# Kernel tuning notes

Hardware: AMD Instinct MI355X
Metric: run time of the kernel (lower is better)

## Reference

```python
import jax, jax.numpy as jnp
import numpy as np
import math

PHI = (1.0 + math.sqrt(5.0)) / 2.0
LUT_SIZE = 4096
D_MODEL = 2048
BATCH = 8192
TWO_PI = 2.0 * math.pi


def lut_sin_cos(theta, sin_table, cos_table):
    """LUT-based sin/cos with linear interpolation over [0, 2*pi)."""
    n = sin_table.shape[0]
    pos = jnp.mod(theta, TWO_PI) * (n / TWO_PI)        # [B, D] in [0, n)
    i0f = jnp.floor(pos)
    frac = pos - i0f
    i0 = i0f.astype(jnp.int32) % n
    i1 = (i0 + 1) % n
    s = sin_table[i0] * (1.0 - frac) + sin_table[i1] * frac
    c = cos_table[i0] * (1.0 - frac) + cos_table[i1] * frac
    return s, c


def setup_inputs() -> dict:
    key = jax.random.key(0)
    ks = jax.random.split(key, 6)
    x_real = jax.random.normal(ks[0], (BATCH, D_MODEL), dtype=jnp.float32)
    x_imag = jax.random.normal(ks[1], (BATCH, D_MODEL), dtype=jnp.float32)
    t = jax.random.uniform(ks[2], (BATCH,), dtype=jnp.float32)
    memory_real = jnp.zeros((BATCH, D_MODEL), dtype=jnp.float32)
    memory_imag = jnp.zeros((BATCH, D_MODEL), dtype=jnp.float32)
    w_trigger = jax.random.normal(ks[3], (D_MODEL,), dtype=jnp.float32) * 0.02
    b_trigger = jnp.zeros((D_MODEL,), dtype=jnp.float32)
    w_state = jax.random.normal(ks[4], (D_MODEL,), dtype=jnp.float32) * 0.02
    b_state = jnp.zeros((D_MODEL,), dtype=jnp.float32)
    k = jnp.asarray(3.0, dtype=jnp.float32)
    grid = jnp.arange(LUT_SIZE, dtype=jnp.float32) * (TWO_PI / LUT_SIZE)
    sin_table = jnp.sin(grid)
    cos_table = jnp.cos(grid)
    return dict(x_real=x_real, x_imag=x_imag, t=t,
                memory_real=memory_real, memory_imag=memory_imag,
                w_trigger=w_trigger, b_trigger=b_trigger,
                w_state=w_state, b_state=b_state, k=k,
                sin_table=sin_table, cos_table=cos_table)


def reference(x_real, x_imag, t, memory_real, memory_imag,
              w_trigger, b_trigger, w_state, b_state, k,
              sin_table, cos_table):
    scale = math.sqrt(x_real.shape[-1])
    t_phi = t[:, None] * PHI                                  # [B, 1]

    # trigger phase
    wl_trigger = 1.0 + jnp.abs(w_trigger)
    theta_tr = x_real / wl_trigger + b_trigger + t_phi
    theta_ti = x_imag / wl_trigger + b_trigger + t_phi
    sin_tr, cos_tr = lut_sin_cos(theta_tr, sin_table, cos_table)
    sin_ti, cos_ti = lut_sin_cos(theta_ti, sin_table, cos_table)
    trigger_real = cos_tr * cos_ti - sin_tr * sin_ti
    trigger_imag = cos_tr * sin_ti + sin_tr * cos_ti

    # interference -> exponential decay gate
    interference_raw = jnp.sum(trigger_real * x_real + trigger_imag * x_imag, axis=-1)
    interference_clamped = jnp.clip(interference_raw / scale, -1.0, 1.0)
    x_inv = (1.0 - interference_clamped) / 2.0
    k_eff = jnp.abs(k) + 0.1
    alpha = jnp.exp(-k_eff * x_inv)[:, None]                  # [B, 1]

    # blend with (detached) memory, then re-evolve
    blended_real = alpha * x_real + (1.0 - alpha) * memory_real
    blended_imag = alpha * x_imag + (1.0 - alpha) * memory_imag
    wl_state = 1.0 + jnp.abs(w_state)
    theta_sr = blended_real / wl_state + b_state + t_phi
    theta_si = blended_imag / wl_state + b_state + t_phi
    sin_sr, cos_sr = lut_sin_cos(theta_sr, sin_table, cos_table)
    sin_si, cos_si = lut_sin_cos(theta_si, sin_table, cos_table)
    evolved_real = cos_sr * cos_si - sin_sr * sin_si
    evolved_imag = cos_sr * sin_si + sin_sr * cos_si
    return evolved_real, evolved_imag
```

## Files before the change

### kernel.cpp

```cpp
#include <hip/hip_runtime.h>

#define DMODEL   2048
#define NTHREADS 256

__device__ __forceinline__ void fast_sincos(float theta, float& s, float& c) {
    const float INV_TWO_PI = 0.15915494309189535f;
    float r  = theta * INV_TWO_PI;
    float rr = r - floorf(r);
#if __has_builtin(__builtin_amdgcn_sinf) && __has_builtin(__builtin_amdgcn_cosf)
    s = __builtin_amdgcn_sinf(rr);
    c = __builtin_amdgcn_cosf(rr);
#else
    s = __sinf(rr * 6.283185307179586f);
    c = __cosf(rr * 6.283185307179586f);
#endif
}

__device__ __forceinline__ float fast_rcp(float x) {
#if __has_builtin(__builtin_amdgcn_rcpf)
    return __builtin_amdgcn_rcpf(x);
#else
    return 1.0f / x;
#endif
}

__global__ __launch_bounds__(NTHREADS)
void liquid_echo_kernel(const float* __restrict__ x_real,
                        const float* __restrict__ x_imag,
                        const float* __restrict__ tvec,
                        const float* __restrict__ memory_real,
                        const float* __restrict__ memory_imag,
                        const float* __restrict__ w_trigger,
                        const float* __restrict__ b_trigger,
                        const float* __restrict__ w_state,
                        const float* __restrict__ b_state,
                        const float* __restrict__ kptr,
                        float* __restrict__ out,
                        size_t imag_off)
{
    __shared__ float red[NTHREADS / 64];

    const int tid = threadIdx.x;
    const int row = blockIdx.x;

    const float t_phi = tvec[row] * 1.6180339887498948f;
    const int c0 = tid * 4;
    const int c1 = (DMODEL / 2) + tid * 4;
    const size_t rb = (size_t)row * DMODEL;

    float4 xr0 = *(const float4*)(x_real + rb + c0);
    float4 xr1 = *(const float4*)(x_real + rb + c1);
    float4 xi0 = *(const float4*)(x_imag + rb + c0);
    float4 xi1 = *(const float4*)(x_imag + rb + c1);
    float4 wt0 = *(const float4*)(w_trigger + c0);
    float4 wt1 = *(const float4*)(w_trigger + c1);
    float4 bt0 = *(const float4*)(b_trigger + c0);
    float4 bt1 = *(const float4*)(b_trigger + c1);

    float xrv[8] = {xr0.x, xr0.y, xr0.z, xr0.w, xr1.x, xr1.y, xr1.z, xr1.w};
    float xiv[8] = {xi0.x, xi0.y, xi0.z, xi0.w, xi1.x, xi1.y, xi1.z, xi1.w};
    float wtv[8] = {wt0.x, wt0.y, wt0.z, wt0.w, wt1.x, wt1.y, wt1.z, wt1.w};
    float btv[8] = {bt0.x, bt0.y, bt0.z, bt0.w, bt1.x, bt1.y, bt1.z, bt1.w};

    float sxy[8];
    float partial = 0.0f;
    #pragma unroll
    for (int j = 0; j < 8; ++j) {
        float iw   = fast_rcp(1.0f + fabsf(wtv[j]));
        float base = btv[j] + t_phi;
        sxy[j]     = xrv[j] + xiv[j];
        float ths  = fmaf(sxy[j], iw, base + base);
        float s, c;
        fast_sincos(ths, s, c);
        partial = fmaf(c, xrv[j], partial);
        partial = fmaf(s, xiv[j], partial);
    }

    float4 mr0 = *(const float4*)(memory_real + rb + c0);
    float4 mr1 = *(const float4*)(memory_real + rb + c1);
    float4 mi0 = *(const float4*)(memory_imag + rb + c0);
    float4 mi1 = *(const float4*)(memory_imag + rb + c1);
    float4 ws0 = *(const float4*)(w_state + c0);
    float4 ws1 = *(const float4*)(w_state + c1);
    float4 bs0 = *(const float4*)(b_state + c0);
    float4 bs1 = *(const float4*)(b_state + c1);

    #pragma unroll
    for (int off = 32; off > 0; off >>= 1)
        partial += __shfl_down(partial, off, 64);
    if ((tid & 63) == 0) red[tid >> 6] = partial;
    __syncthreads();

    float tot   = red[0] + red[1] + red[2] + red[3];
    float ic    = tot * (1.0f / 45.254833995939045f);
    ic          = fminf(1.0f, fmaxf(-1.0f, ic));
    float x_inv = (1.0f - ic) * 0.5f;
    float k_eff = fabsf(kptr[0]) + 0.1f;
    const float alpha = __expf(-k_eff * x_inv);
    const float oma   = 1.0f - alpha;

    float mrv[8] = {mr0.x, mr0.y, mr0.z, mr0.w, mr1.x, mr1.y, mr1.z, mr1.w};
    float miv[8] = {mi0.x, mi0.y, mi0.z, mi0.w, mi1.x, mi1.y, mi1.z, mi1.w};
    float wsv[8] = {ws0.x, ws0.y, ws0.z, ws0.w, ws1.x, ws1.y, ws1.z, ws1.w};
    float bsv[8] = {bs0.x, bs0.y, bs0.z, bs0.w, bs1.x, bs1.y, bs1.z, bs1.w};

    float er[8], ei[8];
    #pragma unroll
    for (int j = 0; j < 8; ++j) {
        float sb   = fmaf(alpha, sxy[j], oma * (mrv[j] + miv[j]));
        float iw   = fast_rcp(1.0f + fabsf(wsv[j]));
        float base = bsv[j] + t_phi;
        float ths  = fmaf(sb, iw, base + base);
        float s, c;
        fast_sincos(ths, s, c);
        er[j] = c;
        ei[j] = s;
    }

    float* outr = out + rb;
    float* outi = out + imag_off + rb;
    *(float4*)(outr + c0) = make_float4(er[0], er[1], er[2], er[3]);
    *(float4*)(outr + c1) = make_float4(er[4], er[5], er[6], er[7]);
    *(float4*)(outi + c0) = make_float4(ei[0], ei[1], ei[2], ei[3]);
    *(float4*)(outi + c1) = make_float4(ei[4], ei[5], ei[6], ei[7]);
}

extern "C" void kernel_launch(void* const* d_in, const int* in_sizes, int n_in,
                              void* d_out, int out_size, void* d_ws, size_t ws_size,
                              hipStream_t stream) {
    const float* x_real      = (const float*)d_in[0];
    const float* x_imag      = (const float*)d_in[1];
    const float* t           = (const float*)d_in[2];
    const float* memory_real = (const float*)d_in[3];
    const float* memory_imag = (const float*)d_in[4];
    const float* w_trigger   = (const float*)d_in[5];
    const float* b_trigger   = (const float*)d_in[6];
    const float* w_state     = (const float*)d_in[7];
    const float* b_state     = (const float*)d_in[8];
    const float* k           = (const float*)d_in[9];
    float* out = (float*)d_out;

    int B = in_sizes[0] / DMODEL;
    size_t imag_off = (size_t)out_size / 2;

    liquid_echo_kernel<<<B, NTHREADS, 0, stream>>>(
        x_real, x_imag, t, memory_real, memory_imag,
        w_trigger, b_trigger, w_state, b_state, k,
        out, imag_off);
}
```

Baseline: 327.0 us.

## Map one wavefront per row with shuffle-only reduction and nontemporal stores

Each 64-lane wavefront now handles a whole row, and a block covers four rows, so the row reduction uses only xor shuffles and needs no shared memory or __syncthreads. Each lane holds 32 elements of x and memory in registers, with outputs written through nontemporal stores. The intent is to remove block-level synchronisation and reduce cache pollution in this bandwidth-bound kernel. The cost is much higher register pressure per thread, which could lower occupancy even with the launch_bounds hint.

```diff
diff --git a/kernel.cpp b/kernel.cpp
--- a/kernel.cpp
+++ b/kernel.cpp
@@ -2,6 +2,10 @@
 
 #define DMODEL   2048
 #define NTHREADS 256
+#define ROWS_PER_BLK 4
+#define CHUNKS   8
+
+typedef float fx4 __attribute__((ext_vector_type(4)));
 
 __device__ __forceinline__ void fast_sincos(float theta, float& s, float& c) {
     const float INV_TWO_PI = 0.15915494309189535f;
@@ -24,7 +28,16 @@
 #endif
 }
 
-__global__ __launch_bounds__(NTHREADS)
+template <typename T>
+__device__ __forceinline__ void nt_store(T v, T* p) {
+#if __has_builtin(__builtin_nontemporal_store)
+    __builtin_nontemporal_store(v, p);
+#else
+    *p = v;
+#endif
+}
+
+__global__ __launch_bounds__(NTHREADS, 4)
 void liquid_echo_kernel(const float* __restrict__ x_real,
                         const float* __restrict__ x_imag,
                         const float* __restrict__ tvec,
@@ -36,93 +49,89 @@
                         const float* __restrict__ b_state,
                         const float* __restrict__ kptr,
                         float* __restrict__ out,
+                        int nrows,
                         size_t imag_off)
 {
-    __shared__ float red[NTHREADS / 64];
-
-    const int tid = threadIdx.x;
-    const int row = blockIdx.x;
+    const int lane = threadIdx.x & 63;
+    const int row  = blockIdx.x * ROWS_PER_BLK + (threadIdx.x >> 6);
+    if (row >= nrows) return;
 
     const float t_phi = tvec[row] * 1.6180339887498948f;
-    const int c0 = tid * 4;
-    const int c1 = (DMODEL / 2) + tid * 4;
-    const size_t rb = (size_t)row * DMODEL;
+    const size_t rb   = (size_t)row * DMODEL;
+    const int cbase   = lane << 2;
 
-    float4 xr0 = *(const float4*)(x_real + rb + c0);
-    float4 xr1 = *(const float4*)(x_real + rb + c1);
-    float4 xi0 = *(const float4*)(x_imag + rb + c0);
-    float4 xi1 = *(const float4*)(x_imag + rb + c1);
-    float4 wt0 = *(const float4*)(w_trigger + c0);
-    float4 wt1 = *(const float4*)(w_trigger + c1);
-    float4 bt0 = *(const float4*)(b_trigger + c0);
-    float4 bt1 = *(const float4*)(b_trigger + c1);
+    fx4 xr[CHUNKS], xi[CHUNKS];
+    #pragma unroll
+    for (int k = 0; k < CHUNKS; ++k) {
+        const int c = (k << 8) + cbase;
+        xr[k] = *(const fx4*)(x_real + rb + c);
+        xi[k] = *(const fx4*)(x_imag + rb + c);
+    }
 
-    float xrv[8] = {xr0.x, xr0.y, xr0.z, xr0.w, xr1.x, xr1.y, xr1.z, xr1.w};
-    float xiv[8] = {xi0.x, xi0.y, xi0.z, xi0.w, xi1.x, xi1.y, xi1.z, xi1.w};
-    float wtv[8] = {wt0.x, wt0.y, wt0.z, wt0.w, wt1.x, wt1.y, wt1.z, wt1.w};
-    float btv[8] = {bt0.x, bt0.y, bt0.z, bt0.w, bt1.x, bt1.y, bt1.z, bt1.w};
-
-    float sxy[8];
+    float sxy[CHUNKS * 4];
     float partial = 0.0f;
     #pragma unroll
-    for (int j = 0; j < 8; ++j) {
-        float iw   = fast_rcp(1.0f + fabsf(wtv[j]));
-        float base = btv[j] + t_phi;
-        sxy[j]     = xrv[j] + xiv[j];
-        float ths  = fmaf(sxy[j], iw, base + base);
-        float s, c;
-        fast_sincos(ths, s, c);
-        partial = fmaf(c, xrv[j], partial);
-        partial = fmaf(s, xiv[j], partial);
+    for (int k = 0; k < CHUNKS; ++k) {
+        const int c = (k << 8) + cbase;
+        const fx4 wt = *(const fx4*)(w_trigger + c);
+        const fx4 bt = *(const fx4*)(b_trigger + c);
+        #pragma unroll
+        for (int j = 0; j < 4; ++j) {
+            float iw   = fast_rcp(1.0f + fabsf(wt[j]));
+            float base = bt[j] + t_phi;
+            float sx   = xr[k][j] + xi[k][j];
+            sxy[k * 4 + j] = sx;
+            float ths  = fmaf(sx, iw, base + base);
+            float s, cc;
+            fast_sincos(ths, s, cc);
+            partial = fmaf(cc, xr[k][j], partial);
+            partial = fmaf(s,  xi[k][j], partial);
+        }
     }
 
-    float4 mr0 = *(const float4*)(memory_real + rb + c0);
-    float4 mr1 = *(const float4*)(memory_real + rb + c1);
-    float4 mi0 = *(const float4*)(memory_imag + rb + c0);
-    float4 mi1 = *(const float4*)(memory_imag + rb + c1);
-    float4 ws0 = *(const float4*)(w_state + c0);
-    float4 ws1 = *(const float4*)(w_state + c1);
-    float4 bs0 = *(const float4*)(b_state + c0);
-    float4 bs1 = *(const float4*)(b_state + c1);
+    fx4 mr[CHUNKS], mi[CHUNKS];
+    #pragma unroll
+    for (int k = 0; k < CHUNKS; ++k) {
+        const int c = (k << 8) + cbase;
+        mr[k] = *(const fx4*)(memory_real + rb + c);
+        mi[k] = *(const fx4*)(memory_imag + rb + c);
+    }
 
     #pragma unroll
     for (int off = 32; off > 0; off >>= 1)
-        partial += __shfl_down(partial, off, 64);
-    if ((tid & 63) == 0) red[tid >> 6] = partial;
-    __syncthreads();
+        partial += __shfl_xor(partial, off, 64);
 
-    float tot   = red[0] + red[1] + red[2] + red[3];
-    float ic    = tot * (1.0f / 45.254833995939045f);
+    float ic    = partial * (1.0f / 45.254833995939045f);
     ic          = fminf(1.0f, fmaxf(-1.0f, ic));
     float x_inv = (1.0f - ic) * 0.5f;
     float k_eff = fabsf(kptr[0]) + 0.1f;
     const float alpha = __expf(-k_eff * x_inv);
     const float oma   = 1.0f - alpha;
 
-    float mrv[8] = {mr0.x, mr0.y, mr0.z, mr0.w, mr1.x, mr1.y, mr1.z, mr1.w};
-    float miv[8] = {mi0.x, mi0.y, mi0.z, mi0.w, mi1.x, mi1.y, mi1.z, mi1.w};
-    float wsv[8] = {ws0.x, ws0.y, ws0.z, ws0.w, ws1.x, ws1.y, ws1.z, ws1.w};
-    float bsv[8] = {bs0.x, bs0.y, bs0.z, bs0.w, bs1.x, bs1.y, bs1.z, bs1.w};
-
-    float er[8], ei[8];
-    #pragma unroll
-    for (int j = 0; j < 8; ++j) {
-        float sb   = fmaf(alpha, sxy[j], oma * (mrv[j] + miv[j]));
-        float iw   = fast_rcp(1.0f + fabsf(wsv[j]));
-        float base = bsv[j] + t_phi;
-        float ths  = fmaf(sb, iw, base + base);
-        float s, c;
-        fast_sincos(ths, s, c);
-        er[j] = c;
-        ei[j] = s;
-    }
-
     float* outr = out + rb;
     float* outi = out + imag_off + rb;
-    *(float4*)(outr + c0) = make_float4(er[0], er[1], er[2], er[3]);
-    *(float4*)(outr + c1) = make_float4(er[4], er[5], er[6], er[7]);
-    *(float4*)(outi + c0) = make_float4(ei[0], ei[1], ei[2], ei[3]);
-    *(float4*)(outi + c1) = make_float4(ei[4], ei[5], ei[6], ei[7]);
+
+    #pragma unroll
+    for (int k = 0; k < CHUNKS; ++k) {
+        const int c = (k << 8) + cbase;
+        const fx4 ws = *(const fx4*)(w_state + c);
+        const fx4 bs = *(const fx4*)(b_state + c);
+        fx4 er, ei;
+        #pragma unroll
+        for (int j = 0; j < 4; ++j) {
+            float smm  = mr[k][j] + mi[k][j];
+            float sb   = fmaf(alpha, sxy[k * 4 + j], oma * smm);
+            float iw   = fast_rcp(1.0f + fabsf(ws[j]));
+            float base = bs[j] + t_phi;
+            float ths  = fmaf(sb, iw, base + base);
+            float s, cc;
+            fast_sincos(ths, s, cc);
+            er[j] = cc;
+            ei[j] = s;
+        }
+        nt_store(er, (fx4*)(outr + c));
+        nt_store(ei, (fx4*)(outi + c));
+    }
 }
 
 extern "C" void kernel_launch(void* const* d_in, const int* in_sizes, int n_in,
@@ -142,9 +151,10 @@
 
     int B = in_sizes[0] / DMODEL;
     size_t imag_off = (size_t)out_size / 2;
+    int grid = (B + ROWS_PER_BLK - 1) / ROWS_PER_BLK;
 
-    liquid_echo_kernel<<<B, NTHREADS, 0, stream>>>(
+    liquid_echo_kernel<<<grid, NTHREADS, 0, stream>>>(
         x_real, x_imag, t, memory_real, memory_imag,
         w_trigger, b_trigger, w_state, b_state, k,
-        out, imag_off);
+        out, B, imag_off);
 }
```

Result: slower. 346.2 us (+5.9%).
